# Kernel tuning notes

Measured on AMD Instinct MI355X. Metric: run time of the kernel, lower is better.

Reference implementation:

```python
import jax, jax.numpy as jnp
import numpy as np

N, E, G = 50000, 800000, 64
F_IN, H, R, C = 64, 64, 3, 10


def setup_inputs() -> dict:
    key = jax.random.key(0)
    ks = jax.random.split(key, 16)
    s = 0.1
    return dict(
        x=jax.random.normal(ks[0], (N, F_IN), jnp.float32),
        edge_index=jax.random.randint(ks[1], (2, E), 0, N, dtype=jnp.int32),
        edge_type=jax.random.randint(ks[2], (E,), 0, R, dtype=jnp.int32),
        graph_batch=jnp.sort(jax.random.randint(ks[3], (N,), 0, G, dtype=jnp.int32)),
        # FiLMConv params (per-relation lin: bias=False; per-relation film: bias=True)
        film_lin_W=jax.random.normal(ks[4], (R, F_IN, H), jnp.float32) * s,
        film_film_W=jax.random.normal(ks[5], (R, F_IN, 2 * H), jnp.float32) * s,
        film_film_b=jnp.zeros((R, 2 * H), jnp.float32),
        skip_W=jax.random.normal(ks[6], (F_IN, H), jnp.float32) * s,
        skip_film_W=jax.random.normal(ks[7], (F_IN, 2 * H), jnp.float32) * s,
        skip_film_b=jnp.zeros((2 * H,), jnp.float32),
        # GATConv params (heads=1, concat=True, lin bias=False, final bias=True)
        gat_W=jax.random.normal(ks[8], (F_IN, H), jnp.float32) * s,
        gat_att_src=jax.random.normal(ks[9], (H,), jnp.float32) * s,
        gat_att_dst=jax.random.normal(ks[10], (H,), jnp.float32) * s,
        gat_b=jnp.zeros((H,), jnp.float32),
        # classifier MLP
        lin_W=jax.random.normal(ks[11], (4 * H, H), jnp.float32) * s,
        lin_b=jnp.zeros((H,), jnp.float32),
        fc_W=jax.random.normal(ks[12], (H, C), jnp.float32) * s,
        fc_b=jnp.zeros((C,), jnp.float32),
    )


def _film_conv(x, edge_index, edge_type, lin_W, film_W, film_b,
               skip_W, skip_film_W, skip_film_b):
    # PyG FiLMConv, aggr='mean' per relation, act=relu.
    n, r, h = x.shape[0], lin_W.shape[0], skip_W.shape[1]
    src, dst = edge_index[0], edge_index[1]
    fs = x @ skip_film_W + skip_film_b                  # [N,2H]; split -> (beta, gamma)
    out = jax.nn.relu(fs[:, h:] * (x @ skip_W) + fs[:, :h])
    xr = jnp.einsum('nd,rdh->rnh', x, lin_W)            # [R,N,H]
    fm = jnp.einsum('nd,rdh->rnh', x, film_W) + film_b[:, None, :]  # [R,N,2H]
    beta, gamma = fm[..., :h], fm[..., h:]
    # each edge uses its own relation's lin/film params
    msg = jax.nn.relu(gamma[edge_type, dst] * xr[edge_type, src] + beta[edge_type, dst])  # [E,H]
    seg = dst * r + edge_type                            # per-(node,relation) mean
    cnt = jax.ops.segment_sum(jnp.ones_like(msg[:, 0]), seg, num_segments=n * r)
    denom = jnp.maximum(cnt[seg], 1.0)
    agg = jax.ops.segment_sum(msg / denom[:, None], dst, num_segments=n)
    return out + agg


def _gat_conv(x, edge_index, W, att_src, att_dst, b):
    # PyG GATConv, heads=1, negative_slope=0.2, add_self_loops=True.
    n = x.shape[0]
    xp = x @ W                                           # [N,H]
    loop = jnp.arange(n, dtype=edge_index.dtype)
    src = jnp.concatenate([edge_index[0], loop])
    dst = jnp.concatenate([edge_index[1], loop])
    e = jax.nn.leaky_relu((xp @ att_src)[src] + (xp @ att_dst)[dst], 0.2)  # [E+N]
    m = jax.ops.segment_max(e, dst, num_segments=n)
    alpha = jnp.exp(e - m[dst])
    denom = jax.ops.segment_sum(alpha, dst, num_segments=n)
    alpha = alpha / denom[dst]
    return jax.ops.segment_sum(alpha[:, None] * xp[src], dst, num_segments=n) + b


def reference(x, edge_index, edge_type, graph_batch,
              film_lin_W, film_film_W, film_film_b, skip_W, skip_film_W, skip_film_b,
              gat_W, gat_att_src, gat_att_dst, gat_b,
              lin_W, lin_b, fc_W, fc_b):
    out1 = jax.nn.relu(_film_conv(x, edge_index, edge_type, film_lin_W, film_film_W,
                                  film_film_b, skip_W, skip_film_W, skip_film_b))
    out2 = jax.nn.relu(_gat_conv(x, edge_index, gat_W, gat_att_src, gat_att_dst, gat_b))
    feats = jnp.concatenate([out1, out2], axis=-1)       # [N,2H]
    g = G
    cnt = jax.ops.segment_sum(jnp.ones_like(feats[:, 0]), graph_batch, num_segments=g)
    mx = jax.ops.segment_max(feats, graph_batch, num_segments=g)
    mx = jnp.where(cnt[:, None] > 0, mx, 0.0)
    mean = jax.ops.segment_sum(feats, graph_batch, num_segments=g) / jnp.maximum(cnt, 1.0)[:, None]
    pooled = jnp.concatenate([mx, mean], axis=-1)        # [G,4H]
    hidden = jax.nn.relu(pooled @ lin_W + lin_b)         # dropout = identity (eval)
    logits = hidden @ fc_W + fc_b
    return jax.nn.log_softmax(logits, axis=-1)
```

## Files before the change

### kernel.cpp

```cpp
#include <hip/hip_runtime.h>
#include <hip/hip_bf16.h>

#define NN 50000
#define EE 800000
#define GG 64
#define RR 3
#define CC 10
#define RPL 16
#define NBG 782
#define NBS 1563

typedef __attribute__((ext_vector_type(8))) short bf16x8;
typedef __attribute__((ext_vector_type(4))) float f32x4;

__device__ inline float leaky02(float x) { return x > 0.f ? x : 0.2f * x; }

__device__ inline void atomicMaxFPos(float* addr, float v) {
  atomicMax((int*)addr, __float_as_int(v));
}

__device__ inline unsigned short f2bf(float f) {
  __hip_bfloat16 b = __float2bfloat16(f);
  return *reinterpret_cast<unsigned short*>(&b);
}
__device__ inline float bf2f(unsigned short u) {
  return __uint_as_float(((unsigned int)u) << 16);
}

__global__ void wpack_k(const float* __restrict__ skip_film_W,
                        const float* __restrict__ skip_W,
                        const float* __restrict__ film_lin_W,
                        const float* __restrict__ film_film_W,
                        const float* __restrict__ gat_W,
                        const float* __restrict__ skip_film_b,
                        const float* __restrict__ film_film_b,
                        unsigned short* __restrict__ Wt,
                        float* __restrict__ bias,
                        float* __restrict__ zbase, int zN4) {
  int tid0 = blockIdx.x * 256 + threadIdx.x;
  float4 z4 = {0.f, 0.f, 0.f, 0.f};
  for (int i = tid0; i < zN4; i += gridDim.x * 256)
    reinterpret_cast<float4*>(zbase)[i] = z4;
  int idx = tid0;
  if (idx >= 832 * 64 + 832) return;
  if (idx >= 832 * 64) {
    int c = idx - 832 * 64;
    float bv = 0.f;
    if (c < 128) bv = skip_film_b[c];
    else if (c >= 384 && c < 768) bv = film_film_b[c - 384];
    bias[c] = bv;
    return;
  }
  int c = idx >> 6, k = idx & 63;
  float v;
  if (c < 128)      v = skip_film_W[k * 128 + c];
  else if (c < 192) v = skip_W[k * 64 + (c - 128)];
  else if (c < 384) { int cc = c - 192, r = cc >> 6, h = cc & 63;
                      v = film_lin_W[(r * 64 + k) * 64 + h]; }
  else if (c < 768) { int cc = c - 384, r = cc >> 7, j = cc & 127;
                      v = film_film_W[(r * 64 + k) * 128 + j]; }
  else              v = gat_W[k * 64 + (c - 768)];
  Wt[idx] = f2bf(v);
}

__global__ __launch_bounds__(256) void fuse_k(const float* __restrict__ X,
    const unsigned short* __restrict__ Wt, const float* __restrict__ bias,
    const float* __restrict__ att_src, const float* __restrict__ att_dst,
    unsigned short* __restrict__ XP, unsigned short* __restrict__ XR,
    unsigned short* __restrict__ Ybg,
    unsigned short* __restrict__ S0b, float* __restrict__ as_,
    float* __restrict__ ad_,
    const int* __restrict__ ei, const int* __restrict__ et,
    int* __restrict__ fill4, unsigned short* __restrict__ sorted) {
  __shared__ __align__(16) unsigned short As[64][72];
  __shared__ __align__(16) unsigned short Bs[128][72];
  const int tid = threadIdx.x;
  const int bid = blockIdx.x;

  if (bid % 3 != 0) {
    int sb = bid - bid / 3 - 1;
    int e = sb * 512 + tid * 2;
    if (e < EE) {
      int2 s2 = *reinterpret_cast<const int2*>(ei + e);
      int2 d2 = *reinterpret_cast<const int2*>(ei + EE + e);
      int2 t2 = *reinterpret_cast<const int2*>(et + e);
      int slot = atomicAdd(&fill4[d2.x * 4 + t2.x], 1);
      if (slot < 32)
        sorted[(size_t)d2.x * 96 + t2.x * 32 + slot] = (unsigned short)s2.x;
      slot = atomicAdd(&fill4[d2.y * 4 + t2.y], 1);
      if (slot < 32)
        sorted[(size_t)d2.y * 96 + t2.y * 32 + slot] = (unsigned short)s2.y;
    }
    return;
  }

  const int row0 = (bid / 3) * 64;
  {
    int r = tid >> 2, c0 = (tid & 3) * 16;
    int gr = row0 + r;
    ushort4 o0 = {0,0,0,0}, o1 = {0,0,0,0}, o2 = {0,0,0,0}, o3 = {0,0,0,0};
    if (gr < NN) {
      const float4* p = reinterpret_cast<const float4*>(X + (size_t)gr * 64 + c0);
      float4 v0 = p[0], v1 = p[1], v2 = p[2], v3 = p[3];
      o0 = {f2bf(v0.x), f2bf(v0.y), f2bf(v0.z), f2bf(v0.w)};
      o1 = {f2bf(v1.x), f2bf(v1.y), f2bf(v1.z), f2bf(v1.w)};
      o2 = {f2bf(v2.x), f2bf(v2.y), f2bf(v2.z), f2bf(v2.w)};
      o3 = {f2bf(v3.x), f2bf(v3.y), f2bf(v3.z), f2bf(v3.w)};
    }
    *reinterpret_cast<ushort4*>(&As[r][c0])      = o0;
    *reinterpret_cast<ushort4*>(&As[r][c0 + 4])  = o1;
    *reinterpret_cast<ushort4*>(&As[r][c0 + 8])  = o2;
    *reinterpret_cast<ushort4*>(&As[r][c0 + 12]) = o3;
  }
  __syncthreads();

  const int w = tid >> 6, lane = tid & 63;
  const int m = lane & 15, q = lane >> 4;
  bf16x8 a0 = *reinterpret_cast<const bf16x8*>(&As[16 * w + m][q * 8]);
  bf16x8 a1 = *reinterpret_cast<const bf16x8*>(&As[16 * w + m][32 + q * 8]);
  const int rbase = row0 + 16 * w + q * 4;

  f32x4 t0[8], t1[4], t6[4];

  for (int tile = 0; tile < 7; tile++) {
    __syncthreads();
    int col0 = tile * 128;
    int width = (tile == 6) ? 64 : 128;
    {
      int c = tid >> 1, half = (tid & 1) * 32;
      if (c < width) {
        int gc = col0 + c;
        const uint4* p = reinterpret_cast<const uint4*>(Wt + (size_t)gc * 64 + half);
        uint4 v0 = p[0], v1 = p[1], v2 = p[2], v3 = p[3];
        *reinterpret_cast<uint4*>(&Bs[c][half])      = v0;
        *reinterpret_cast<uint4*>(&Bs[c][half + 8])  = v1;
        *reinterpret_cast<uint4*>(&Bs[c][half + 16]) = v2;
        *reinterpret_cast<uint4*>(&Bs[c][half + 24]) = v3;
      }
    }
    __syncthreads();
    #pragma unroll
    for (int ct = 0; ct < 8; ct++) {
      if (tile == 6 && ct >= 4) continue;
      bf16x8 b0 = *reinterpret_cast<const bf16x8*>(&Bs[ct * 16 + m][q * 8]);
      bf16x8 b1 = *reinterpret_cast<const bf16x8*>(&Bs[ct * 16 + m][32 + q * 8]);
      f32x4 acc = {0.f, 0.f, 0.f, 0.f};
      acc = __builtin_amdgcn_mfma_f32_16x16x32_bf16(a0, b0, acc, 0, 0, 0);
      acc = __builtin_amdgcn_mfma_f32_16x16x32_bf16(a1, b1, acc, 0, 0, 0);
      if (tile == 0) { t0[ct] = acc; continue; }
      if (tile == 1 && ct < 4) { t1[ct] = acc; continue; }
      if (tile == 6) t6[ct] = acc;
      int colm = ct * 16 + m;
      float bv = (tile >= 3 && tile <= 5) ? bias[col0 + colm] : 0.f;
      #pragma unroll
      for (int rg = 0; rg < 4; rg++) {
        int gr = rbase + rg;
        if (gr >= NN) continue;
        float v = acc[rg];
        if (tile == 1) {
          XR[(size_t)gr * 64 + (colm - 64)] = f2bf(v);
        } else if (tile == 2) {
          if (ct < 4) XR[((size_t)NN + gr) * 64 + colm]            = f2bf(v);
          else        XR[((size_t)2 * NN + gr) * 64 + (colm - 64)] = f2bf(v);
        } else if (tile <= 5) {
          Ybg[(size_t)gr * 384 + (col0 - 384) + colm] = f2bf(v + bv);
        } else {
          XP[(size_t)gr * 64 + colm] = f2bf(v);
        }
      }
    }
  }

  float pa[4] = {0.f, 0.f, 0.f, 0.f}, pd[4] = {0.f, 0.f, 0.f, 0.f};
  #pragma unroll
  for (int j = 0; j < 4; j++) {
    int h = 16 * j + m;
    float bb = bias[h];
    float bg = bias[64 + h];
    float asv = att_src[h];
    float adv = att_dst[h];
    #pragma unroll
    for (int rg = 0; rg < 4; rg++) {
      float so = fmaxf((t0[4 + j][rg] + bg) * t1[j][rg] + (t0[j][rg] + bb), 0.f);
      int gr = rbase + rg;
      if (gr < NN) S0b[(size_t)gr * 64 + h] = f2bf(so);
      pa[rg] += t6[j][rg] * asv;
      pd[rg] += t6[j][rg] * adv;
    }
  }
  #pragma unroll
  for (int ofs = 1; ofs < 16; ofs <<= 1) {
    #pragma unroll
    for (int rg = 0; rg < 4; rg++) {
      pa[rg] += __shfl_xor(pa[rg], ofs);
      pd[rg] += __shfl_xor(pd[rg], ofs);
    }
  }
  if (m == 0) {
    #pragma unroll
    for (int rg = 0; rg < 4; rg++) {
      int gr = rbase + rg;
      if (gr < NN) { as_[gr] = pa[rg]; ad_[gr] = pd[rg]; }
    }
  }
}

#define RPN 16

__global__ __launch_bounds__(256) void dst_k(const unsigned short* __restrict__ sorted,
    const int* __restrict__ fill4, const unsigned short* __restrict__ XP,
    const unsigned short* __restrict__ XR,
    const unsigned short* __restrict__ Ybg,
    const unsigned short* __restrict__ S0b,
    const float* __restrict__ as_, const float* __restrict__ ad_,
    const float* __restrict__ gat_b, const int* __restrict__ gb,
    float* __restrict__ pmax, float* __restrict__ psum,
    int* __restrict__ gstart, int* __restrict__ gend) {
  __shared__ int   s_pk[4][96];
  __shared__ float s_w [4][96];
  __shared__ int   s_d [4][4];
  __shared__ int   s_g[4];
  __shared__ float s_ad[4];
  __shared__ __align__(16) unsigned short s_rows[64][128];
  float* s_val = (float*)&s_rows[0][0];

  const int tid = threadIdx.x;
  const int wid = tid >> 6, h = tid & 63;
  const int n0 = blockIdx.x * 4;
  const int n  = n0 + wid;

  size_t rep = (size_t)(blockIdx.x & (RPL - 1)) * GG * 128;
  pmax += rep; psum += rep;

  if (tid < 16) {
    int wd = tid >> 2, t = tid & 3;
    if (t < 3) {
      int d = fill4[(n0 + wd) * 4 + t];
      s_d[wd][t] = d > 32 ? 32 : d;
    } else {
      s_g[wd]  = gb[n0 + wd];
      s_ad[wd] = ad_[n0 + wd];
    }
  }
  __syncthreads();

  for (int i = tid; i < 512; i += 256) {
    int wd = i >> 7, s = i & 127;
    if (s < 96) {
      int tt = s >> 5, j = s & 31;
      if (j < s_d[wd][tt]) {
        int cidx = (tt == 0) ? j
                 : (tt == 1) ? s_d[wd][0] + j
                             : s_d[wd][0] + s_d[wd][1] + j;
        int src = sorted[(size_t)(n0 + wd) * 96 + s];
        s_pk[wd][cidx] = src;
        s_w[wd][cidx]  = leaky02(as_[src] + s_ad[wd]);
      }
    }
  }
  __syncthreads();

  const int d0 = s_d[wid][0], d1 = s_d[wid][1], d2 = s_d[wid][2];
  const int sB = d0 + d1;
  const int deg = sB + d2;
  const float adn = s_ad[wid];
  float es = leaky02(as_[n] + adn);

  bool v1 = h < deg;
  bool v2 = h + 64 < deg;
  float e1 = v1 ? s_w[wid][h]      : -1e30f;
  float e2 = v2 ? s_w[wid][64 + h] : -1e30f;
  float mg = fmaxf(fmaxf(e1, e2), es);
  #pragma unroll
  for (int ofs = 1; ofs < 64; ofs <<= 1) mg = fmaxf(mg, __shfl_xor(mg, ofs));
  float w1 = v1 ? __expf(e1 - mg) : 0.f;
  float w2 = v2 ? __expf(e2 - mg) : 0.f;
  if (v1) s_w[wid][h] = w1;
  if (v2) s_w[wid][64 + h] = w2;
  float den = w1 + w2;
  #pragma unroll
  for (int ofs = 1; ofs < 64; ofs <<= 1) den += __shfl_xor(den, ofs);
  float ws = __expf(es - mg);
  den += ws;

  const float i0 = 1.f / (float)(d0 > 1 ? d0 : 1);
  const float i1 = 1.f / (float)(d1 > 1 ? d1 : 1);
  const float i2 = 1.f / (float)(d2 > 1 ? d2 : 1);
  const unsigned short* ybg = Ybg + (size_t)n * 384;
  const float b0p = bf2f(ybg[h])       * i0, g0p = bf2f(ybg[64 + h])  * i0;
  const float b1p = bf2f(ybg[128 + h]) * i1, g1p = bf2f(ybg[192 + h]) * i1;
  const float b2p = bf2f(ybg[256 + h]) * i2, g2p = bf2f(ybg[320 + h]) * i2;

  float S = ws * bf2f(XP[(size_t)n * 64 + h]);
  float f = 0.f;

  const int grp16 = tid >> 4, lane16 = tid & 15;
  int kA[4], kB[4], kD[4];
  #pragma unroll
  for (int k = 0; k < 4; k++) {
    kA[k] = s_d[k][0];
    kB[k] = kA[k] + s_d[k][1];
    kD[k] = kB[k] + s_d[k][2];
  }
  int dmax = max(max(kD[0], kD[1]), max(kD[2], kD[3]));
  int rounds = (dmax + RPN - 1) / RPN;

  for (int r = 0; r < rounds; r++) {
    int e0 = r * RPN;
    #pragma unroll
    for (int k = 0; k < 4; k++) {
      int jj = e0 + grp16;
      if (jj < kD[k]) {
        int src = s_pk[k][jj];
        int t = jj < kA[k] ? 0 : (jj < kB[k] ? 1 : 2);
        const unsigned short* row = (lane16 < 8)
            ? XP + (size_t)src * 64 + lane16 * 8
            : XR + ((size_t)t * NN + src) * 64 + (lane16 - 8) * 8;
        uint4 v = *reinterpret_cast<const uint4*>(row);
        *reinterpret_cast<uint4*>(&s_rows[16 * k + grp16][lane16 * 8]) = v;
      }
    }
    __syncthreads();
    const unsigned short* rowp = &s_rows[wid * RPN][0];
    int hi0 = min(e0 + RPN, d0);
    for (int i = e0; i < hi0; i++) {
      float wj = s_w[wid][i];
      int sr = i - e0;
      float xp = bf2f(rowp[sr * 128 + h]);
      float xr = bf2f(rowp[sr * 128 + 64 + h]);
      S += wj * xp;
      f += fmaxf(g0p * xr + b0p, 0.f);
    }
    int lo1 = max(e0, d0), hi1 = min(e0 + RPN, sB);
    for (int i = lo1; i < hi1; i++) {
      float wj = s_w[wid][i];
      int sr = i - e0;
      float xp = bf2f(rowp[sr * 128 + h]);
      float xr = bf2f(rowp[sr * 128 + 64 + h]);
      S += wj * xp;
      f += fmaxf(g1p * xr + b1p, 0.f);
    }
    int lo2 = max(e0, sB), hi2 = min(e0 + RPN, deg);
    for (int i = lo2; i < hi2; i++) {
      float wj = s_w[wid][i];
      int sr = i - e0;
      float xp = bf2f(rowp[sr * 128 + h]);
      float xr = bf2f(rowp[sr * 128 + 64 + h]);
      S += wj * xp;
      f += fmaxf(g2p * xr + b2p, 0.f);
    }
    __syncthreads();
  }

  float o1 = fmaxf(bf2f(S0b[(size_t)n * 64 + h]) + f, 0.f);
  float o2 = fmaxf(S / den + gat_b[h], 0.f);

  s_val[wid * 128 + h]      = o1;
  s_val[wid * 128 + 64 + h] = o2;
  if (h == 0) {
    int g = s_g[wid];
    if (n == 0 || gb[n - 1] != g)      gstart[g] = n;
    if (n == NN - 1 || gb[n + 1] != g) gend[g] = n;
  }
  __syncthreads();
  if (tid < 128) {
    int fch = tid;
    int curg = s_g[0];
    float v0 = s_val[fch];
    float mx = v0, sm = v0;
    #pragma unroll
    for (int j = 1; j < 4; j++) {
      float v = s_val[j * 128 + fch];
      if (s_g[j] == curg) { mx = fmaxf(mx, v); sm += v; }
      else {
        atomicMaxFPos(&pmax[curg * 128 + fch], mx);
        atomicAdd(&psum[curg * 128 + fch], sm);
        curg = s_g[j]; mx = v; sm = v;
      }
    }
    atomicMaxFPos(&pmax[curg * 128 + fch], mx);
    atomicAdd(&psum[curg * 128 + fch], sm);
  }
}

__global__ __launch_bounds__(256) void head_k(const float* __restrict__ pmax,
    const float* __restrict__ psum, const int* __restrict__ gstart,
    const int* __restrict__ gend,
    const float* __restrict__ lin_W, const float* __restrict__ lin_b,
    const float* __restrict__ fc_W, const float* __restrict__ fc_b,
    float* __restrict__ out) {
  __shared__ float p[256];
  __shared__ float ph[4][64];
  __shared__ float hid[64];
  __shared__ float lg[CC];
  __shared__ float lse;
  int g = blockIdx.x, t = threadIdx.x;
  int s = gstart[g], e = gend[g];
  int cnt = (s <= e && s < NN && s >= 0) ? (e - s + 1) : 0;
  float invc = 1.f / (float)(cnt > 1 ? cnt : 1);
  if (t < 128) {
    float mx = 0.f;
    #pragma unroll
    for (int r = 0; r < RPL; r++)
      mx = fmaxf(mx, pmax[((size_t)r * GG + g) * 128 + t]);
    p[t] = mx;
  } else {
    int f = t - 128;
    float sm = 0.f;
    #pragma unroll
    for (int r = 0; r < RPL; r++)
      sm += psum[((size_t)r * GG + g) * 128 + f];
    p[t] = sm * invc;
  }
  __syncthreads();
  {
    int part = t >> 6, tt = t & 63;
    float acc = 0.f;
    int k0 = part * 64;
    for (int k = k0; k < k0 + 64; k++) acc += p[k] * lin_W[k * 64 + tt];
    ph[part][tt] = acc;
  }
  __syncthreads();
  if (t < 64) {
    float a = lin_b[t] + ph[0][t] + ph[1][t] + ph[2][t] + ph[3][t];
    hid[t] = fmaxf(a, 0.f);
  }
  __syncthreads();
  if (t < CC) {
    float a = fc_b[t];
    for (int k = 0; k < 64; k++) a += hid[k] * fc_W[k * CC + t];
    lg[t] = a;
  }
  __syncthreads();
  if (t == 0) {
    float mx = lg[0];
    for (int i = 1; i < CC; i++) mx = fmaxf(mx, lg[i]);
    float sum = 0.f;
    for (int i = 0; i < CC; i++) sum += expf(lg[i] - mx);
    lse = mx + logf(sum);
  }
  __syncthreads();
  if (t < CC) out[g * CC + t] = lg[t] - lse;
}

extern "C" void kernel_launch(void* const* d_in, const int* in_sizes, int n_in,
                              void* d_out, int out_size, void* d_ws, size_t ws_size,
                              hipStream_t stream) {
  const float* x            = (const float*)d_in[0];
  const int*   edge_index   = (const int*)d_in[1];
  const int*   edge_type    = (const int*)d_in[2];
  const int*   graph_batch  = (const int*)d_in[3];
  const float* film_lin_W   = (const float*)d_in[4];
  const float* film_film_W  = (const float*)d_in[5];
  const float* film_film_b  = (const float*)d_in[6];
  const float* skip_W       = (const float*)d_in[7];
  const float* skip_film_W  = (const float*)d_in[8];
  const float* skip_film_b  = (const float*)d_in[9];
  const float* gat_W        = (const float*)d_in[10];
  const float* att_src      = (const float*)d_in[11];
  const float* att_dst      = (const float*)d_in[12];
  const float* gat_b        = (const float*)d_in[13];
  const float* lin_W        = (const float*)d_in[14];
  const float* lin_b        = (const float*)d_in[15];
  const float* fc_W         = (const float*)d_in[16];
  const float* fc_b         = (const float*)d_in[17];
  float* out                = (float*)d_out;

  float* ws = (float*)d_ws;
  const size_t N = NN, G = GG;
  size_t oXP     = 0;
  size_t oXR     = N * 32;
  size_t oYbg    = oXR + N * 96;
  size_t oS0     = oYbg + N * 192;
  size_t oAs     = oS0 + N * 32;
  size_t oAd     = oAs + N;
  size_t oWt     = oAd + N;
  size_t oBias   = oWt + 832 * 32;
  size_t oPmax   = oBias + 832;
  size_t oPsum   = oPmax + (size_t)RPL * G * 128;
  size_t oGend   = oPsum + (size_t)RPL * G * 128;
  size_t oFill   = oGend + G;
  size_t oGstart = oFill + N * 4;
  size_t oSorted = oGstart + G;

  unsigned short* XP  = (unsigned short*)(ws + oXP);
  unsigned short* XR  = (unsigned short*)(ws + oXR);
  unsigned short* Ybg = (unsigned short*)(ws + oYbg);
  unsigned short* S0b = (unsigned short*)(ws + oS0);
  float* as_    = ws + oAs;
  float* ad_    = ws + oAd;
  unsigned short* Wt  = (unsigned short*)(ws + oWt);
  float* bias   = ws + oBias;
  float* pmax   = ws + oPmax;
  float* psum   = ws + oPsum;
  int*   gend   = (int*)(ws + oGend);
  int*   fill4  = (int*)(ws + oFill);
  int*   gstart = (int*)(ws + oGstart);
  unsigned short* sorted = (unsigned short*)(ws + oSorted);

  int zN4 = (int)((oGstart - oPmax) / 4);

  wpack_k<<<212, 256, 0, stream>>>(skip_film_W, skip_W, film_lin_W,
                                   film_film_W, gat_W, skip_film_b,
                                   film_film_b, Wt, bias, pmax, zN4);
  fuse_k<<<NBG + NBS, 256, 0, stream>>>(x, Wt, bias, att_src, att_dst,
                                        XP, XR, Ybg, S0b, as_, ad_,
                                        edge_index, edge_type, fill4, sorted);
  dst_k<<<NN / 4, 256, 0, stream>>>(sorted, fill4, XP, XR, Ybg, S0b, as_, ad_,
                                    gat_b, graph_batch, pmax, psum,
                                    gstart, gend);
  head_k<<<GG, 256, 0, stream>>>(pmax, psum, gstart, gend,
                                 lin_W, lin_b, fc_W, fc_b, out);
}
```

Measured before the change: 235.9 us.

## Fuse all stages into one cooperative persistent kernel with grid syncs

Merges weight packing, the bf16 GEMM plus edge bucketing stage, the per-destination aggregation stage and the classifier head into a single cooperative kernel. The stages are separated by grid.sync and blocks loop over virtual block indices. The goal is to remove the launch gaps and the idle tails between the four kernel launches. In exchange it adds grid-wide barrier cost and limits the grid to the resident block count. It also changes scheduling, since the formerly interleaved GEMM and scatter blocks now share persistent blocks.

```diff
diff --git a/kernel.cpp b/kernel.cpp
--- a/kernel.cpp
+++ b/kernel.cpp
@@ -1,5 +1,6 @@
 #include <hip/hip_runtime.h>
 #include <hip/hip_bf16.h>
+#include <hip/hip_cooperative_groups.h>
 
 #define NN 50000
 #define EE 800000
@@ -9,9 +10,14 @@
 #define RPL 16
 #define NBG 782
 #define NBS 1563
+#define NV1 (NBG + NBS)
+#define ND4 (NN / 4)
+#define WTN (832 * 64 + 832)
+#define RPN 16
 
 typedef __attribute__((ext_vector_type(8))) short bf16x8;
 typedef __attribute__((ext_vector_type(4))) float f32x4;
+namespace cg = cooperative_groups;
 
 __device__ inline float leaky02(float x) { return x > 0.f ? x : 0.2f * x; }
 
@@ -25,6 +31,417 @@
 }
 __device__ inline float bf2f(unsigned short u) {
   return __uint_as_float(((unsigned int)u) << 16);
+}
+
+__device__ inline float wpack_val(int idx,
+    const float* skip_film_W, const float* skip_W, const float* film_lin_W,
+    const float* film_film_W, const float* gat_W) {
+  int c = idx >> 6, k = idx & 63;
+  if (c < 128)      return skip_film_W[k * 128 + c];
+  if (c < 192)      return skip_W[k * 64 + (c - 128)];
+  if (c < 384) { int cc = c - 192, r = cc >> 6, h = cc & 63;
+                 return film_lin_W[(r * 64 + k) * 64 + h]; }
+  if (c < 768) { int cc = c - 384, r = cc >> 7, j = cc & 127;
+                 return film_film_W[(r * 64 + k) * 128 + j]; }
+  return gat_W[k * 64 + (c - 768)];
+}
+
+__global__ __launch_bounds__(256) void mega_k(
+    const float* __restrict__ X, const int* __restrict__ ei,
+    const int* __restrict__ et, const int* __restrict__ gb,
+    const float* __restrict__ skip_film_W, const float* __restrict__ skip_W,
+    const float* __restrict__ film_lin_W, const float* __restrict__ film_film_W,
+    const float* __restrict__ gat_W, const float* __restrict__ skip_film_b,
+    const float* __restrict__ film_film_b, const float* __restrict__ att_src,
+    const float* __restrict__ att_dst, const float* __restrict__ gat_b,
+    const float* __restrict__ lin_W, const float* __restrict__ lin_b,
+    const float* __restrict__ fc_W, const float* __restrict__ fc_b,
+    unsigned short* __restrict__ XP, unsigned short* __restrict__ XR,
+    unsigned short* __restrict__ Ybg, unsigned short* __restrict__ S0b,
+    float* __restrict__ as_, float* __restrict__ ad_,
+    unsigned short* __restrict__ Wt, float* __restrict__ bias,
+    float* __restrict__ pmax, float* __restrict__ psum,
+    int* __restrict__ gend, int* __restrict__ fill4,
+    int* __restrict__ gstart, unsigned short* __restrict__ sorted,
+    float* __restrict__ zbase, int zN4, float* __restrict__ out) {
+  cg::grid_group grid = cg::this_grid();
+  __shared__ __align__(16) unsigned char smem[20480];
+  const int tid = threadIdx.x;
+  const int bid = blockIdx.x;
+  const int nb  = gridDim.x;
+  const int gsz = nb * 256;
+
+  {
+    float4 z4 = {0.f, 0.f, 0.f, 0.f};
+    for (int i = bid * 256 + tid; i < zN4; i += gsz)
+      reinterpret_cast<float4*>(zbase)[i] = z4;
+    for (int idx = bid * 256 + tid; idx < WTN; idx += gsz) {
+      if (idx >= 832 * 64) {
+        int c = idx - 832 * 64;
+        float bv = 0.f;
+        if (c < 128) bv = skip_film_b[c];
+        else if (c >= 384 && c < 768) bv = film_film_b[c - 384];
+        bias[c] = bv;
+      } else {
+        Wt[idx] = f2bf(wpack_val(idx, skip_film_W, skip_W, film_lin_W,
+                                 film_film_W, gat_W));
+      }
+    }
+  }
+  grid.sync();
+
+  {
+    unsigned short (*As)[72] = (unsigned short(*)[72])smem;
+    unsigned short (*Bs)[72] = (unsigned short(*)[72])(smem + 9216);
+    for (int vb = bid; vb < NV1; vb += nb) {
+      __syncthreads();
+      if (vb % 3 != 0) {
+        int sb = vb - vb / 3 - 1;
+        int e = sb * 512 + tid * 2;
+        if (e < EE) {
+          int2 s2 = *reinterpret_cast<const int2*>(ei + e);
+          int2 d2 = *reinterpret_cast<const int2*>(ei + EE + e);
+          int2 t2 = *reinterpret_cast<const int2*>(et + e);
+          int slot = atomicAdd(&fill4[d2.x * 4 + t2.x], 1);
+          if (slot < 32)
+            sorted[(size_t)d2.x * 96 + t2.x * 32 + slot] = (unsigned short)s2.x;
+          slot = atomicAdd(&fill4[d2.y * 4 + t2.y], 1);
+          if (slot < 32)
+            sorted[(size_t)d2.y * 96 + t2.y * 32 + slot] = (unsigned short)s2.y;
+        }
+        continue;
+      }
+      const int row0 = (vb / 3) * 64;
+      {
+        int r = tid >> 2, c0 = (tid & 3) * 16;
+        int gr = row0 + r;
+        ushort4 o0 = {0,0,0,0}, o1 = {0,0,0,0}, o2 = {0,0,0,0}, o3 = {0,0,0,0};
+        if (gr < NN) {
+          const float4* p = reinterpret_cast<const float4*>(X + (size_t)gr * 64 + c0);
+          float4 v0 = p[0], v1 = p[1], v2 = p[2], v3 = p[3];
+          o0 = {f2bf(v0.x), f2bf(v0.y), f2bf(v0.z), f2bf(v0.w)};
+          o1 = {f2bf(v1.x), f2bf(v1.y), f2bf(v1.z), f2bf(v1.w)};
+          o2 = {f2bf(v2.x), f2bf(v2.y), f2bf(v2.z), f2bf(v2.w)};
+          o3 = {f2bf(v3.x), f2bf(v3.y), f2bf(v3.z), f2bf(v3.w)};
+        }
+        *reinterpret_cast<ushort4*>(&As[r][c0])      = o0;
+        *reinterpret_cast<ushort4*>(&As[r][c0 + 4])  = o1;
+        *reinterpret_cast<ushort4*>(&As[r][c0 + 8])  = o2;
+        *reinterpret_cast<ushort4*>(&As[r][c0 + 12]) = o3;
+      }
+      __syncthreads();
+      const int w = tid >> 6, lane = tid & 63;
+      const int m = lane & 15, q = lane >> 4;
+      bf16x8 a0 = *reinterpret_cast<const bf16x8*>(&As[16 * w + m][q * 8]);
+      bf16x8 a1 = *reinterpret_cast<const bf16x8*>(&As[16 * w + m][32 + q * 8]);
+      const int rbase = row0 + 16 * w + q * 4;
+      f32x4 t0[8], t1[4], t6[4];
+
+      for (int tile = 0; tile < 13; tile++) {
+        __syncthreads();
+        int col0 = tile * 64;
+        {
+          int c = tid >> 2, qq = (tid & 3) * 16;
+          const uint4* p = reinterpret_cast<const uint4*>(
+              Wt + (size_t)(col0 + c) * 64 + qq);
+          uint4 v0 = p[0], v1 = p[1];
+          *reinterpret_cast<uint4*>(&Bs[c][qq])     = v0;
+          *reinterpret_cast<uint4*>(&Bs[c][qq + 8]) = v1;
+        }
+        __syncthreads();
+        #pragma unroll
+        for (int ct = 0; ct < 4; ct++) {
+          bf16x8 b0 = *reinterpret_cast<const bf16x8*>(&Bs[ct * 16 + m][q * 8]);
+          bf16x8 b1 = *reinterpret_cast<const bf16x8*>(&Bs[ct * 16 + m][32 + q * 8]);
+          f32x4 acc = {0.f, 0.f, 0.f, 0.f};
+          acc = __builtin_amdgcn_mfma_f32_16x16x32_bf16(a0, b0, acc, 0, 0, 0);
+          acc = __builtin_amdgcn_mfma_f32_16x16x32_bf16(a1, b1, acc, 0, 0, 0);
+          if (tile == 0) { t0[ct] = acc; continue; }
+          if (tile == 1) { t0[4 + ct] = acc; continue; }
+          if (tile == 2) { t1[ct] = acc; continue; }
+          if (tile == 12) t6[ct] = acc;
+          int cm = ct * 16 + m;
+          float bv = (tile >= 6 && tile <= 11) ? bias[col0 + cm] : 0.f;
+          #pragma unroll
+          for (int rg = 0; rg < 4; rg++) {
+            int gr = rbase + rg;
+            if (gr >= NN) continue;
+            float v = acc[rg];
+            if (tile <= 5) {
+              XR[((size_t)(tile - 3) * NN + gr) * 64 + cm] = f2bf(v);
+            } else if (tile <= 11) {
+              Ybg[(size_t)gr * 384 + (tile - 6) * 64 + cm] = f2bf(v + bv);
+            } else {
+              XP[(size_t)gr * 64 + cm] = f2bf(v);
+            }
+          }
+        }
+      }
+
+      float pa[4] = {0.f, 0.f, 0.f, 0.f}, pd[4] = {0.f, 0.f, 0.f, 0.f};
+      #pragma unroll
+      for (int j = 0; j < 4; j++) {
+        int h = 16 * j + m;
+        float bb = bias[h];
+        float bg = bias[64 + h];
+        float asv = att_src[h];
+        float adv = att_dst[h];
+        #pragma unroll
+        for (int rg = 0; rg < 4; rg++) {
+          float so = fmaxf((t0[4 + j][rg] + bg) * t1[j][rg] + (t0[j][rg] + bb), 0.f);
+          int gr = rbase + rg;
+          if (gr < NN) S0b[(size_t)gr * 64 + h] = f2bf(so);
+          pa[rg] += t6[j][rg] * asv;
+          pd[rg] += t6[j][rg] * adv;
+        }
+      }
+      #pragma unroll
+      for (int ofs = 1; ofs < 16; ofs <<= 1) {
+        #pragma unroll
+        for (int rg = 0; rg < 4; rg++) {
+          pa[rg] += __shfl_xor(pa[rg], ofs);
+          pd[rg] += __shfl_xor(pd[rg], ofs);
+        }
+      }
+      if (m == 0) {
+        #pragma unroll
+        for (int rg = 0; rg < 4; rg++) {
+          int gr = rbase + rg;
+          if (gr < NN) { as_[gr] = pa[rg]; ad_[gr] = pd[rg]; }
+        }
+      }
+    }
+  }
+  __threadfence();
+  grid.sync();
+
+  {
+    unsigned short (*s_rows)[128] = (unsigned short(*)[128])smem;
+    int   (*s_pk)[96] = (int(*)[96])(smem + 16384);
+    float (*s_w)[96]  = (float(*)[96])(smem + 17920);
+    int   (*s_d)[4]   = (int(*)[4])(smem + 19456);
+    int*   s_g        = (int*)(smem + 19520);
+    float* s_ad       = (float*)(smem + 19536);
+    float* s_val      = (float*)smem;
+
+    const int wid = tid >> 6, h = tid & 63;
+    const int grp16 = tid >> 4, lane16 = tid & 15;
+
+    for (int vb = bid; vb < ND4; vb += nb) {
+      __syncthreads();
+      const int n0 = vb * 4;
+      const int n  = n0 + wid;
+      size_t rep = (size_t)(vb & (RPL - 1)) * GG * 128;
+      float* pm = pmax + rep;
+      float* ps = psum + rep;
+
+      if (tid < 16) {
+        int wd = tid >> 2, t = tid & 3;
+        if (t < 3) {
+          int d = fill4[(n0 + wd) * 4 + t];
+          s_d[wd][t] = d > 32 ? 32 : d;
+        } else {
+          s_g[wd]  = gb[n0 + wd];
+          s_ad[wd] = ad_[n0 + wd];
+        }
+      }
+      __syncthreads();
+
+      for (int i = tid; i < 512; i += 256) {
+        int wd = i >> 7, s = i & 127;
+        if (s < 96) {
+          int tt = s >> 5, j = s & 31;
+          if (j < s_d[wd][tt]) {
+            int cidx = (tt == 0) ? j
+                     : (tt == 1) ? s_d[wd][0] + j
+                                 : s_d[wd][0] + s_d[wd][1] + j;
+            int src = sorted[(size_t)(n0 + wd) * 96 + s];
+            s_pk[wd][cidx] = src;
+            s_w[wd][cidx]  = leaky02(as_[src] + s_ad[wd]);
+          }
+        }
+      }
+      __syncthreads();
+
+      const int d0 = s_d[wid][0], d1 = s_d[wid][1], d2 = s_d[wid][2];
+      const int sB = d0 + d1;
+      const int deg = sB + d2;
+      const float adn = s_ad[wid];
+      float es = leaky02(as_[n] + adn);
+
+      bool v1 = h < deg;
+      bool v2 = h + 64 < deg;
+      float e1 = v1 ? s_w[wid][h]      : -1e30f;
+      float e2 = v2 ? s_w[wid][64 + h] : -1e30f;
+      float mg = fmaxf(fmaxf(e1, e2), es);
+      #pragma unroll
+      for (int ofs = 1; ofs < 64; ofs <<= 1) mg = fmaxf(mg, __shfl_xor(mg, ofs));
+      float w1 = v1 ? __expf(e1 - mg) : 0.f;
+      float w2 = v2 ? __expf(e2 - mg) : 0.f;
+      if (v1) s_w[wid][h] = w1;
+      if (v2) s_w[wid][64 + h] = w2;
+      float den = w1 + w2;
+      #pragma unroll
+      for (int ofs = 1; ofs < 64; ofs <<= 1) den += __shfl_xor(den, ofs);
+      float wsf = __expf(es - mg);
+      den += wsf;
+
+      const float i0 = 1.f / (float)(d0 > 1 ? d0 : 1);
+      const float i1 = 1.f / (float)(d1 > 1 ? d1 : 1);
+      const float i2 = 1.f / (float)(d2 > 1 ? d2 : 1);
+      const unsigned short* ybg = Ybg + (size_t)n * 384;
+      const float b0p = bf2f(ybg[h])       * i0, g0p = bf2f(ybg[64 + h])  * i0;
+      const float b1p = bf2f(ybg[128 + h]) * i1, g1p = bf2f(ybg[192 + h]) * i1;
+      const float b2p = bf2f(ybg[256 + h]) * i2, g2p = bf2f(ybg[320 + h]) * i2;
+
+      float S = wsf * bf2f(XP[(size_t)n * 64 + h]);
+      float f = 0.f;
+
+      int kA[4], kB[4], kD[4];
+      #pragma unroll
+      for (int k = 0; k < 4; k++) {
+        kA[k] = s_d[k][0];
+        kB[k] = kA[k] + s_d[k][1];
+        kD[k] = kB[k] + s_d[k][2];
+      }
+      int dmax = max(max(kD[0], kD[1]), max(kD[2], kD[3]));
+      int rounds = (dmax + RPN - 1) / RPN;
+
+      for (int r = 0; r < rounds; r++) {
+        int e0 = r * RPN;
+        #pragma unroll
+        for (int k = 0; k < 4; k++) {
+          int jj = e0 + grp16;
+          if (jj < kD[k]) {
+            int src = s_pk[k][jj];
+            int t = jj < kA[k] ? 0 : (jj < kB[k] ? 1 : 2);
+            const unsigned short* row = (lane16 < 8)
+                ? XP + (size_t)src * 64 + lane16 * 8
+                : XR + ((size_t)t * NN + src) * 64 + (lane16 - 8) * 8;
+            uint4 v = *reinterpret_cast<const uint4*>(row);
+            *reinterpret_cast<uint4*>(&s_rows[16 * k + grp16][lane16 * 8]) = v;
+          }
+        }
+        __syncthreads();
+        const unsigned short* rowp = &s_rows[wid * RPN][0];
+        int hi0 = min(e0 + RPN, d0);
+        for (int i = e0; i < hi0; i++) {
+          float wj = s_w[wid][i];
+          int sr = i - e0;
+          float xp = bf2f(rowp[sr * 128 + h]);
+          float xr = bf2f(rowp[sr * 128 + 64 + h]);
+          S += wj * xp;
+          f += fmaxf(g0p * xr + b0p, 0.f);
+        }
+        int lo1 = max(e0, d0), hi1 = min(e0 + RPN, sB);
+        for (int i = lo1; i < hi1; i++) {
+          float wj = s_w[wid][i];
+          int sr = i - e0;
+          float xp = bf2f(rowp[sr * 128 + h]);
+          float xr = bf2f(rowp[sr * 128 + 64 + h]);
+          S += wj * xp;
+          f += fmaxf(g1p * xr + b1p, 0.f);
+        }
+        int lo2 = max(e0, sB), hi2 = min(e0 + RPN, deg);
+        for (int i = lo2; i < hi2; i++) {
+          float wj = s_w[wid][i];
+          int sr = i - e0;
+          float xp = bf2f(rowp[sr * 128 + h]);
+          float xr = bf2f(rowp[sr * 128 + 64 + h]);
+          S += wj * xp;
+          f += fmaxf(g2p * xr + b2p, 0.f);
+        }
+        __syncthreads();
+      }
+
+      float o1 = fmaxf(bf2f(S0b[(size_t)n * 64 + h]) + f, 0.f);
+      float o2 = fmaxf(S / den + gat_b[h], 0.f);
+
+      s_val[wid * 128 + h]      = o1;
+      s_val[wid * 128 + 64 + h] = o2;
+      if (h == 0) {
+        int g = s_g[wid];
+        if (n == 0 || gb[n - 1] != g)      gstart[g] = n;
+        if (n == NN - 1 || gb[n + 1] != g) gend[g] = n;
+      }
+      __syncthreads();
+      if (tid < 128) {
+        int fch = tid;
+        int curg = s_g[0];
+        float v0 = s_val[fch];
+        float mx = v0, sm = v0;
+        #pragma unroll
+        for (int j = 1; j < 4; j++) {
+          float v = s_val[j * 128 + fch];
+          if (s_g[j] == curg) { mx = fmaxf(mx, v); sm += v; }
+          else {
+            atomicMaxFPos(&pm[curg * 128 + fch], mx);
+            atomicAdd(&ps[curg * 128 + fch], sm);
+            curg = s_g[j]; mx = v; sm = v;
+          }
+        }
+        atomicMaxFPos(&pm[curg * 128 + fch], mx);
+        atomicAdd(&ps[curg * 128 + fch], sm);
+      }
+    }
+  }
+  __threadfence();
+  grid.sync();
+
+  if (bid < GG) {
+    float* p        = (float*)smem;
+    float (*ph)[64] = (float(*)[64])(smem + 1024);
+    float* hid      = (float*)(smem + 2048);
+    float* lg       = (float*)(smem + 2304);
+    float* lsep     = (float*)(smem + 2352);
+    int g = bid, t = tid;
+    int s = gstart[g], e = gend[g];
+    int cnt = (s <= e && s < NN && s >= 0) ? (e - s + 1) : 0;
+    float invc = 1.f / (float)(cnt > 1 ? cnt : 1);
+    if (t < 128) {
+      float mx = 0.f;
+      #pragma unroll
+      for (int r = 0; r < RPL; r++)
+        mx = fmaxf(mx, pmax[((size_t)r * GG + g) * 128 + t]);
+      p[t] = mx;
+    } else {
+      int f = t - 128;
+      float sm = 0.f;
+      #pragma unroll
+      for (int r = 0; r < RPL; r++)
+        sm += psum[((size_t)r * GG + g) * 128 + f];
+      p[t] = sm * invc;
+    }
+    __syncthreads();
+    {
+      int part = t >> 6, tt = t & 63;
+      float acc = 0.f;
+      int k0 = part * 64;
+      for (int k = k0; k < k0 + 64; k++) acc += p[k] * lin_W[k * 64 + tt];
+      ph[part][tt] = acc;
+    }
+    __syncthreads();
+    if (t < 64) {
+      float a = lin_b[t] + ph[0][t] + ph[1][t] + ph[2][t] + ph[3][t];
+      hid[t] = fmaxf(a, 0.f);
+    }
+    __syncthreads();
+    if (t < CC) {
+      float a = fc_b[t];
+      for (int k = 0; k < 64; k++) a += hid[k] * fc_W[k * CC + t];
+      lg[t] = a;
+    }
+    __syncthreads();
+    if (t == 0) {
+      float mx = lg[0];
+      for (int i = 1; i < CC; i++) mx = fmaxf(mx, lg[i]);
+      float sum = 0.f;
+      for (int i = 0; i < CC; i++) sum += expf(lg[i] - mx);
+      *lsep = mx + logf(sum);
+    }
+    __syncthreads();
+    if (t < CC) out[g * CC + t] = lg[t] - *lsep;
+  }
 }
 
 __global__ void wpack_k(const float* __restrict__ skip_film_W,
@@ -42,7 +459,7 @@
   for (int i = tid0; i < zN4; i += gridDim.x * 256)
     reinterpret_cast<float4*>(zbase)[i] = z4;
   int idx = tid0;
-  if (idx >= 832 * 64 + 832) return;
+  if (idx >= WTN) return;
   if (idx >= 832 * 64) {
     int c = idx - 832 * 64;
     float bv = 0.f;
@@ -51,16 +468,8 @@
     bias[c] = bv;
     return;
   }
-  int c = idx >> 6, k = idx & 63;
-  float v;
-  if (c < 128)      v = skip_film_W[k * 128 + c];
-  else if (c < 192) v = skip_W[k * 64 + (c - 128)];
-  else if (c < 384) { int cc = c - 192, r = cc >> 6, h = cc & 63;
-                      v = film_lin_W[(r * 64 + k) * 64 + h]; }
-  else if (c < 768) { int cc = c - 384, r = cc >> 7, j = cc & 127;
-                      v = film_film_W[(r * 64 + k) * 128 + j]; }
-  else              v = gat_W[k * 64 + (c - 768)];
-  Wt[idx] = f2bf(v);
+  Wt[idx] = f2bf(wpack_val(idx, skip_film_W, skip_W, film_lin_W,
+                           film_film_W, gat_W));
 }
 
 __global__ __launch_bounds__(256) void fuse_k(const float* __restrict__ X,
@@ -205,8 +614,6 @@
   }
 }
 
-#define RPN 16
-
 __global__ __launch_bounds__(256) void dst_k(const unsigned short* __restrict__ sorted,
     const int* __restrict__ fill4, const unsigned short* __restrict__ XP,
     const unsigned short* __restrict__ XR,
@@ -219,7 +626,7 @@
   __shared__ int   s_pk[4][96];
   __shared__ float s_w [4][96];
   __shared__ int   s_d [4][4];
-  __shared__ int   s_g[4];
+  __shared__ int s_g[4];
   __shared__ float s_ad[4];
   __shared__ __align__(16) unsigned short s_rows[64][128];
   float* s_val = (float*)&s_rows[0][0];
@@ -498,11 +905,46 @@
   int*   gstart = (int*)(ws + oGstart);
   unsigned short* sorted = (unsigned short*)(ws + oSorted);
 
+  float* zbase = pmax;
   int zN4 = (int)((oGstart - oPmax) / 4);
+
+  static int s_mode = 0;
+  static int s_nblk = 0;
+  if (s_mode == 0) {
+    int bpc = 0;
+    hipError_t oe = hipOccupancyMaxActiveBlocksPerMultiprocessor(
+        &bpc, reinterpret_cast<const void*>(mega_k), 256, 0);
+    if (oe == hipSuccess && bpc >= 1) {
+      s_nblk = bpc * 256;
+      if (s_nblk > 2048) s_nblk = 2048;
+      s_mode = 1;
+    } else {
+      s_mode = 2;
+    }
+  }
+
+  if (s_mode == 1) {
+    void* args[] = {
+      (void*)&x, (void*)&edge_index, (void*)&edge_type, (void*)&graph_batch,
+      (void*)&skip_film_W, (void*)&skip_W, (void*)&film_lin_W,
+      (void*)&film_film_W, (void*)&gat_W, (void*)&skip_film_b,
+      (void*)&film_film_b, (void*)&att_src, (void*)&att_dst, (void*)&gat_b,
+      (void*)&lin_W, (void*)&lin_b, (void*)&fc_W, (void*)&fc_b,
+      (void*)&XP, (void*)&XR, (void*)&Ybg, (void*)&S0b, (void*)&as_,
+      (void*)&ad_, (void*)&Wt, (void*)&bias, (void*)&pmax, (void*)&psum,
+      (void*)&gend, (void*)&fill4, (void*)&gstart, (void*)&sorted,
+      (void*)&zbase, (void*)&zN4, (void*)&out
+    };
+    hipError_t le = hipLaunchCooperativeKernel(
+        reinterpret_cast<void*>(mega_k), dim3(s_nblk), dim3(256),
+        args, 0, stream);
+    if (le == hipSuccess) return;
+    s_mode = 2;
+  }
 
   wpack_k<<<212, 256, 0, stream>>>(skip_film_W, skip_W, film_lin_W,
                                    film_film_W, gat_W, skip_film_b,
-                                   film_film_b, Wt, bias, pmax, zN4);
+                                   film_film_b, Wt, bias, zbase, zN4);
   fuse_k<<<NBG + NBS, 256, 0, stream>>>(x, Wt, bias, att_src, att_dst,
                                         XP, XR, Ybg, S0b, as_, ad_,
                                         edge_index, edge_type, fill4, sorted);
```

Measured after the change: 714.0 us. +202.7%, slower.
